# Performance work log

Hardware: AMD Instinct MI355X
Metric: run time of the kernel (lower is better)

Reference implementation:

```python
import jax, jax.numpy as jnp
import numpy as np

B, T, D_MODEL, HEAD_DIM = 8, 2048, 1024, 128


def setup_inputs() -> dict:
    key = jax.random.key(0)
    k1, k2, k3, k4 = jax.random.split(key, 4)
    scale = 1.0 / np.sqrt(D_MODEL)
    return {
        "x": jax.random.normal(k1, (B, T, D_MODEL), dtype=jnp.float32),
        "Wq": jax.random.normal(k2, (HEAD_DIM, D_MODEL), dtype=jnp.float32) * scale,
        "Wk": jax.random.normal(k3, (HEAD_DIM, D_MODEL), dtype=jnp.float32) * scale,
        "Wv": jax.random.normal(k4, (HEAD_DIM, D_MODEL), dtype=jnp.float32) * scale,
    }


def reference(x, Wq, Wk, Wv) -> jnp.ndarray:
    # x: [B, T, C]; torch Linear(no bias): y = x @ W.T, W: [head_dim, d_model]
    q = jnp.einsum("btc,hc->bth", x, Wq)  # [B, T, H]
    k = jnp.einsum("btc,hc->bth", x, Wk)
    v = jnp.einsum("btc,hc->bth", x, Wv)
    head_dim = Wq.shape[0]
    scores = jnp.einsum("bqh,bkh->bqk", q, k) / jnp.sqrt(jnp.float32(head_dim))  # [B, T, T]
    T_ = x.shape[1]
    causal = jnp.tril(jnp.ones((T_, T_), dtype=bool))
    scores = jnp.where(causal, scores, -jnp.inf)
    probs = jax.nn.softmax(scores, axis=-1)
    # dropout is identity at inference (eval mode)
    out = jnp.einsum("bqk,bkh->bqh", probs, v)  # [B, T, head_dim]
    return out
```

## Files before the change

kernel.cpp:

```cpp
#include <hip/hip_runtime.h>
#include <hip/hip_bf16.h>
#include <math.h>

#define T_ 2048
#define C_ 1024
#define H_ 128
#define NB 8
#define WN 131072
#define SC 0.08838834764831845f

typedef __attribute__((ext_vector_type(8))) short bf16x8;
typedef __attribute__((ext_vector_type(8))) unsigned short u16x8;
typedef __attribute__((ext_vector_type(4))) float f32x4;

#define MFMA16(a,b,c) __builtin_amdgcn_mfma_f32_16x16x32_bf16((a),(b),(c),0,0,0)

__device__ __forceinline__ unsigned short f2bf(float f) {
    union { float f; unsigned u; } v; v.f = f;
    unsigned r = v.u + 0x7fffu + ((v.u >> 16) & 1u);
    return (unsigned short)(r >> 16);
}
__device__ __forceinline__ float bf2f(unsigned short u) {
    union { unsigned u; float f; } v; v.u = ((unsigned)u) << 16; return v.f;
}
__device__ __forceinline__ unsigned pk2bf(float a, float b) {
    __hip_bfloat162 h = __float22bfloat162_rn(float2{a, b});
    union { __hip_bfloat162 h; unsigned u; } v; v.h = h; return v.u;
}
__device__ __forceinline__ void gld16(void* lds, const void* g) {
    __builtin_amdgcn_global_load_lds(
        (const __attribute__((address_space(1))) unsigned*)g,
        (__attribute__((address_space(3))) unsigned*)lds, 16, 0, 0);
}

__global__ __launch_bounds__(256) void wconv(const float* __restrict__ Wq,
                                             const float* __restrict__ Wk,
                                             const float* __restrict__ Wv,
                                             unsigned short* __restrict__ Wb) {
    int e = (blockIdx.x * 256 + threadIdx.x) * 8;
    int which = e >> 17;
    int off = e & (WN - 1);
    const float* src = (which == 0) ? Wq : (which == 1 ? Wk : Wv);
    float s = (which == 0) ? SC : 1.0f;
    const float4* p = (const float4*)(src + off);
    float4 a = p[0], b = p[1];
    uint4 o = { pk2bf(a.x * s, a.y * s), pk2bf(a.z * s, a.w * s),
                pk2bf(b.x * s, b.y * s), pk2bf(b.z * s, b.w * s) };
    *(uint4*)(Wb + e) = o;
}

__global__ __launch_bounds__(256, 2) void proj(const float* __restrict__ x,
                                               const unsigned short* __restrict__ Wb,
                                               unsigned short* __restrict__ Q,
                                               unsigned short* __restrict__ K,
                                               unsigned short* __restrict__ V) {
    __shared__ unsigned short Xs[2][32][40];
    __shared__ unsigned short Ws[2][384][32];

    const int tid  = threadIdx.x;
    const int wave = tid >> 6, lane = tid & 63;
    const int quad = lane >> 4, l16 = lane & 15;
    const int m0   = blockIdx.x * 32;

    f32x4 acc[2][6];
    #pragma unroll
    for (int i = 0; i < 2; i++)
        #pragma unroll
        for (int j = 0; j < 6; j++) acc[i][j] = {0.f, 0.f, 0.f, 0.f};

    const int xrow = tid >> 3, xc4 = (tid & 7) * 4;
    const float* xg = x + (size_t)(m0 + xrow) * C_ + xc4;
    const unsigned short* wg = Wb + (size_t)(wave * 96 + (lane >> 2)) * C_
                               + (size_t)(((lane & 3) ^ ((lane >> 3) & 3)) * 8);

    #define STAGE(buf, kc) do {                                                   \
        _Pragma("unroll")                                                         \
        for (int rb = 0; rb < 6; rb++)                                            \
            gld16(&Ws[buf][wave * 96 + rb * 16][0],                               \
                  wg + (size_t)rb * 16 * C_ + (kc));                              \
        float4 f = *(const float4*)(xg + (kc));                                   \
        *(uint2*)&Xs[buf][xrow][xc4] = uint2{ pk2bf(f.x, f.y), pk2bf(f.z, f.w) }; \
    } while (0)

    STAGE(0, 0);
    for (int it = 0; it < 32; it++) {
        __syncthreads();
        if (it < 31) { STAGE((it + 1) & 1, (it + 1) * 32); }
        const int buf = it & 1;
        bf16x8 af[2];
        af[0] = *(bf16x8*)&Xs[buf][l16][quad * 8];
        af[1] = *(bf16x8*)&Xs[buf][16 + l16][quad * 8];
        const int rsw = (l16 >> 1) & 3;
        #pragma unroll
        for (int nf = 0; nf < 6; nf++) {
            int row = wave * 96 + nf * 16 + l16;
            bf16x8 bq = *(bf16x8*)&Ws[buf][row][(quad ^ rsw) * 8];
            acc[0][nf] = MFMA16(af[0], bq, acc[0][nf]);
            acc[1][nf] = MFMA16(af[1], bq, acc[1][nf]);
        }
    }
    #undef STAGE

    #pragma unroll
    for (int nf = 0; nf < 6; nf++) {
        int nb = wave * 96 + nf * 16;
        int which = nb >> 7;
        unsigned short* dst = (which == 0) ? Q : (which == 1 ? K : V);
        int c = (nb & 127) + l16;
        #pragma unroll
        for (int mf = 0; mf < 2; mf++)
            #pragma unroll
            for (int r = 0; r < 4; r++)
                dst[(size_t)(m0 + mf * 16 + quad * 4 + r) * H_ + c] = f2bf(acc[mf][nf][r]);
    }
}

__global__ __launch_bounds__(256, 3) void attn(const unsigned short* __restrict__ Qg,
                                               const unsigned short* __restrict__ Kg,
                                               const unsigned short* __restrict__ Vg,
                                               unsigned short* __restrict__ Ob,
                                               float* __restrict__ Ml) {
    const int bx = blockIdx.x;
    const int s  = bx & 7, qt = 31 - (bx >> 3);
    const int b  = blockIdx.y;
    const int qbase = qt * 64, kstart = s * 256;
    if (kstart > qbase) return;
    const int kend  = (kstart + 256 < qbase + 64) ? kstart + 256 : qbase + 64;
    const int niter = (kend - kstart) >> 6;

    __shared__ unsigned short Ks[4][64][32];
    __shared__ unsigned short Vt[128 * 64];
    __shared__ unsigned short Ps[4][16][64];

    const int tid = threadIdx.x, wave = tid >> 6, lane = tid & 63;
    const int quad = lane >> 4, l16 = lane & 15;
    const size_t base = (size_t)b * T_ * H_;

    const unsigned short* ksrc = Kg + base + (size_t)(kstart + (lane >> 2)) * H_ + wave * 32 + (lane & 3) * 8;
    #pragma unroll
    for (int p = 0; p < 4; p++) gld16(&Ks[wave][p * 16][0], ksrc + (size_t)p * 16 * H_);
    const unsigned short* vsrc = Vg + base + (size_t)(kstart + wave * 8 + quad * 2) * H_ + l16 * 8;
    u16x8 vr[2][2];
    vr[0][0] = *(const u16x8*)vsrc;             vr[0][1] = *(const u16x8*)(vsrc + H_);
    vr[1][0] = *(const u16x8*)(vsrc + 32 * H_); vr[1][1] = *(const u16x8*)(vsrc + 33 * H_);

    bf16x8 qf[4];
    const unsigned short* qp = Qg + base + (size_t)(qbase + wave * 16 + l16) * H_ + quad * 8;
    #pragma unroll
    for (int kk = 0; kk < 4; kk++) qf[kk] = *(const bf16x8*)(qp + kk * 32);

    f32x4 o[8];
    #pragma unroll
    for (int i = 0; i < 8; i++) o[i] = {0.f, 0.f, 0.f, 0.f};
    float m_i = -INFINITY, l_i = 0.f;
    const int swz = (l16 & 7) << 3;
    const int qg = qbase + wave * 16 + l16;

    __syncthreads();

    #pragma unroll
    for (int g = 0; g < 2; g++) {
        int t0 = wave * 8 + g * 32 + quad * 2;
        int t8 = t0 >> 3;
        #pragma unroll
        for (int j = 0; j < 8; j++) {
            int h = l16 * 8 + j;
            unsigned pk = (unsigned)(unsigned short)vr[g][0][j] | ((unsigned)(unsigned short)vr[g][1][j] << 16);
            int blk = (t8 ^ (h & 7) ^ ((h >> 3) & 7)) & 7;
            *(unsigned*)&Vt[h * 64 + blk * 8 + (t0 & 7)] = pk;
        }
    }

    for (int kt = 0; ; kt++) {
        const int kbase = kstart + kt * 64;
        f32x4 st[4];
        #pragma unroll
        for (int nf = 0; nf < 4; nf++) st[nf] = {0.f, 0.f, 0.f, 0.f};
        #pragma unroll
        for (int kk = 0; kk < 4; kk++)
            #pragma unroll
            for (int nf = 0; nf < 4; nf++) {
                bf16x8 kfr = *(bf16x8*)&Ks[kk][nf * 16 + l16][quad * 8];
                st[nf] = MFMA16(kfr, qf[kk], st[nf]);
            }
        if (kbase + 64 > qbase) {
            #pragma unroll
            for (int nf = 0; nf < 4; nf++) {
                int kg = kbase + nf * 16 + quad * 4;
                #pragma unroll
                for (int r = 0; r < 4; r++)
                    if (kg + r > qg) st[nf][r] = -INFINITY;
            }
        }
        float mx = st[0][0];
        #pragma unroll
        for (int nf = 0; nf < 4; nf++)
            #pragma unroll
            for (int r = 0; r < 4; r++) mx = fmaxf(mx, st[nf][r]);
        mx = fmaxf(mx, __shfl_xor(mx, 16, 64));
        mx = fmaxf(mx, __shfl_xor(mx, 32, 64));
        float mnew = fmaxf(m_i, mx);
        float al = __expf(m_i - mnew);
        m_i = mnew;
        float rs = 0.f;
        #pragma unroll
        for (int nf = 0; nf < 4; nf++)
            #pragma unroll
            for (int r = 0; r < 4; r++) {
                float e = __expf(st[nf][r] - mnew);
                st[nf][r] = e; rs += e;
            }
        rs += __shfl_xor(rs, 16, 64);
        rs += __shfl_xor(rs, 32, 64);
        l_i = al * l_i + rs;
        #pragma unroll
        for (int nf = 0; nf < 4; nf++) {
            uint2 pk = { pk2bf(st[nf][0], st[nf][1]), pk2bf(st[nf][2], st[nf][3]) };
            *(uint2*)&Ps[wave][l16][(nf * 16 + quad * 4) ^ swz] = pk;
        }
        float a0 = __shfl(al, quad * 4 + 0, 64), a1 = __shfl(al, quad * 4 + 1, 64);
        float a2 = __shfl(al, quad * 4 + 2, 64), a3 = __shfl(al, quad * 4 + 3, 64);
        #pragma unroll
        for (int i = 0; i < 8; i++) {
            o[i][0] *= a0; o[i][1] *= a1; o[i][2] *= a2; o[i][3] *= a3;
        }
        __syncthreads();

        const bool more = (kt + 1 < niter);
        if (more) {
            ksrc += 64 * H_;
            #pragma unroll
            for (int p = 0; p < 4; p++) gld16(&Ks[wave][p * 16][0], ksrc + (size_t)p * 16 * H_);
            vsrc += 64 * H_;
            vr[0][0] = *(const u16x8*)vsrc;             vr[0][1] = *(const u16x8*)(vsrc + H_);
            vr[1][0] = *(const u16x8*)(vsrc + 32 * H_); vr[1][1] = *(const u16x8*)(vsrc + 33 * H_);
        }
        bf16x8 pa0 = *(bf16x8*)&Ps[wave][l16][(quad * 8) ^ swz];
        bf16x8 pa1 = *(bf16x8*)&Ps[wave][l16][(32 + quad * 8) ^ swz];
        #pragma unroll
        for (int nf = 0; nf < 8; nf++) {
            int h = nf * 16 + l16;
            int ex = (h & 7) ^ ((h >> 3) & 7);
            bf16x8 v0 = *(bf16x8*)&Vt[h * 64 + ((quad ^ ex) & 7) * 8];
            bf16x8 v1 = *(bf16x8*)&Vt[h * 64 + (((quad + 4) ^ ex) & 7) * 8];
            o[nf] = MFMA16(pa0, v0, o[nf]);
            o[nf] = MFMA16(pa1, v1, o[nf]);
        }
        if (!more) break;
        __syncthreads();
        #pragma unroll
        for (int g = 0; g < 2; g++) {
            int t0 = wave * 8 + g * 32 + quad * 2;
            int t8 = t0 >> 3;
            #pragma unroll
            for (int j = 0; j < 8; j++) {
                int h = l16 * 8 + j;
                unsigned pk = (unsigned)(unsigned short)vr[g][0][j] | ((unsigned)(unsigned short)vr[g][1][j] << 16);
                int blk = (t8 ^ (h & 7) ^ ((h >> 3) & 7)) & 7;
                *(unsigned*)&Vt[h * 64 + blk * 8 + (t0 & 7)] = pk;
            }
        }
    }

    const int g2 = qt >> 2;
    const int Pq = 2 * g2 * (g2 + 1) + (qt & 3) * (g2 + 1);
    const int slot = (Pq + s) * NB + b;
    float lq[4];
    #pragma unroll
    for (int r = 0; r < 4; r++) lq[r] = __shfl(l_i, quad * 4 + r, 64);
    const size_t obase = (size_t)slot * 64 * 128;
    #pragma unroll
    for (int r = 0; r < 4; r++) {
        float invl = 1.0f / lq[r];
        #pragma unroll
        for (int nf = 0; nf < 8; nf++)
            Ob[obase + (size_t)(wave * 16 + quad * 4 + r) * 128 + nf * 16 + l16] = f2bf(o[nf][r] * invl);
    }
    if (lane < 16) {
        int ridx = slot * 64 + wave * 16 + l16;
        Ml[ridx * 2]     = m_i;
        Ml[ridx * 2 + 1] = l_i;
    }
}

__global__ __launch_bounds__(256) void merge(const unsigned short* __restrict__ Ob,
                                             const float* __restrict__ Ml,
                                             float* __restrict__ out) {
    const int qt = blockIdx.x, b = blockIdx.y;
    const int g = qt >> 2;
    const int Pq = 2 * g * (g + 1) + (qt & 3) * (g + 1);
    const int ns = g + 1;
    const int tid = threadIdx.x;
    const int row = tid >> 2, c0 = (tid & 3) * 32;

    float mv[8], lv[8], mg = -INFINITY;
    for (int s2 = 0; s2 < ns; s2++) {
        int slot = (Pq + s2) * NB + b;
        mv[s2] = Ml[(slot * 64 + row) * 2];
        lv[s2] = Ml[(slot * 64 + row) * 2 + 1];
        mg = fmaxf(mg, mv[s2]);
    }
    float L = 0.f, w[8];
    for (int s2 = 0; s2 < ns; s2++) { w[s2] = lv[s2] * __expf(mv[s2] - mg); L += w[s2]; }
    float inv = 1.0f / L;

    float accv[32];
    #pragma unroll
    for (int i = 0; i < 32; i++) accv[i] = 0.f;
    for (int s2 = 0; s2 < ns; s2++) {
        int slot = (Pq + s2) * NB + b;
        const unsigned short* op = Ob + ((size_t)(slot * 64 + row)) * 128 + c0;
        #pragma unroll
        for (int cc = 0; cc < 4; cc++) {
            u16x8 v = *(const u16x8*)(op + cc * 8);
            #pragma unroll
            for (int j = 0; j < 8; j++) accv[cc * 8 + j] += w[s2] * bf2f(v[j]);
        }
    }
    float* od = out + ((size_t)(b * T_ + qt * 64 + row)) * 128 + c0;
    #pragma unroll
    for (int cc = 0; cc < 8; cc++) {
        float4 w4 = { accv[cc*4] * inv, accv[cc*4+1] * inv, accv[cc*4+2] * inv, accv[cc*4+3] * inv };
        *(float4*)(od + cc * 4) = w4;
    }
}

extern "C" void kernel_launch(void* const* d_in, const int* in_sizes, int n_in,
                              void* d_out, int out_size, void* d_ws, size_t ws_size,
                              hipStream_t stream) {
    const float* x  = (const float*)d_in[0];
    const float* Wq = (const float*)d_in[1];
    const float* Wk = (const float*)d_in[2];
    const float* Wv = (const float*)d_in[3];

    char* ws = (char*)d_ws;
    unsigned short* Wb = (unsigned short*)ws;
    unsigned short* Q  = (unsigned short*)(ws + (size_t) 1 * (1u << 20));
    unsigned short* K  = (unsigned short*)(ws + (size_t) 5 * (1u << 20));
    unsigned short* V  = (unsigned short*)(ws + (size_t) 9 * (1u << 20));
    unsigned short* Ob = (unsigned short*)(ws + (size_t)13 * (1u << 20));
    float*          Ml = (float*)(ws + (size_t)32 * (1u << 20));
    float* out = (float*)d_out;

    hipLaunchKernelGGL(wconv, dim3(192), dim3(256), 0, stream, Wq, Wk, Wv, Wb);
    hipLaunchKernelGGL(proj,  dim3(512), dim3(256), 0, stream, x, Wb, Q, K, V);
    hipLaunchKernelGGL(attn,  dim3(256, NB), dim3(256), 0, stream, Q, K, V, Ob, Ml);
    hipLaunchKernelGGL(merge, dim3(32, NB), dim3(256), 0, stream, Ob, Ml, out);
}
```

Measured before the change: 181.7 us.

## Retile QKV projection to 64x192 blocks with K=64 steps and deferred X conversion

The projection kernel now gives each block a 64-row by 192-column output tile, using a 2x2 wave grid and 64-wide K slices with XOR-swizzled shared memory. This halves the number of K iterations, and each loaded X tile is reused across more output columns per wave. The fp32 X loads are issued before the MFMAs and converted and stored to shared memory afterwards, so their global latency overlaps compute. In exchange, each block re-reads X for both column halves, and it uses more shared memory and registers, which may reduce occupancy.

Measured after the change: 175.0 us. 3.7% less time.

```diff
diff --git a/kernel.cpp b/kernel.cpp
--- a/kernel.cpp
+++ b/kernel.cpp
@@ -54,13 +54,15 @@
                                                unsigned short* __restrict__ Q,
                                                unsigned short* __restrict__ K,
                                                unsigned short* __restrict__ V) {
-    __shared__ unsigned short Xs[2][32][40];
-    __shared__ unsigned short Ws[2][384][32];
+    __shared__ unsigned short Xs[2][64][64];
+    __shared__ unsigned short Ws[2][192][64];
 
     const int tid  = threadIdx.x;
     const int wave = tid >> 6, lane = tid & 63;
     const int quad = lane >> 4, l16 = lane & 15;
-    const int m0   = blockIdx.x * 32;
+    const int wm   = wave >> 1, wn = wave & 1;
+    const int m0   = (blockIdx.x >> 1) * 64;
+    const int n0   = (blockIdx.x & 1) * 192;
 
     f32x4 acc[2][6];
     #pragma unroll
@@ -68,42 +70,62 @@
         #pragma unroll
         for (int j = 0; j < 6; j++) acc[i][j] = {0.f, 0.f, 0.f, 0.f};
 
-    const int xrow = tid >> 3, xc4 = (tid & 7) * 4;
-    const float* xg = x + (size_t)(m0 + xrow) * C_ + xc4;
-    const unsigned short* wg = Wb + (size_t)(wave * 96 + (lane >> 2)) * C_
-                               + (size_t)(((lane & 3) ^ ((lane >> 3) & 3)) * 8);
-
-    #define STAGE(buf, kc) do {                                                   \
+    const int xrow = tid >> 2, xcg = tid & 3;
+    const float* xg = x + (size_t)(m0 + xrow) * C_ + xcg * 16;
+    const int xk = xrow & 7;
+    const unsigned short* wg = Wb + (size_t)(n0 + wave * 48 + (lane >> 3)) * C_
+                               + (size_t)(((lane & 7) ^ (lane >> 3)) * 8);
+
+    float4 xr0, xr1, xr2, xr3;
+    #define ISSUE(buf, kc) do {                                                   \
         _Pragma("unroll")                                                         \
-        for (int rb = 0; rb < 6; rb++)                                            \
-            gld16(&Ws[buf][wave * 96 + rb * 16][0],                               \
-                  wg + (size_t)rb * 16 * C_ + (kc));                              \
-        float4 f = *(const float4*)(xg + (kc));                                   \
-        *(uint2*)&Xs[buf][xrow][xc4] = uint2{ pk2bf(f.x, f.y), pk2bf(f.z, f.w) }; \
+        for (int i = 0; i < 6; i++)                                               \
+            gld16(&Ws[buf][wave * 48 + i * 8][0], wg + (size_t)i * 8 * C_ + (kc));\
+        const float* xp = xg + (kc);                                              \
+        xr0 = *(const float4*)xp;        xr1 = *(const float4*)(xp + 4);          \
+        xr2 = *(const float4*)(xp + 8);  xr3 = *(const float4*)(xp + 12);         \
     } while (0)
 
-    STAGE(0, 0);
-    for (int it = 0; it < 32; it++) {
+    #define XWRITE(buf) do {                                                      \
+        uint4 u0 = { pk2bf(xr0.x, xr0.y), pk2bf(xr0.z, xr0.w),                    \
+                     pk2bf(xr1.x, xr1.y), pk2bf(xr1.z, xr1.w) };                  \
+        uint4 u1 = { pk2bf(xr2.x, xr2.y), pk2bf(xr2.z, xr2.w),                    \
+                     pk2bf(xr3.x, xr3.y), pk2bf(xr3.z, xr3.w) };                  \
+        *(uint4*)&Xs[buf][xrow][((2 * xcg)     ^ xk) * 8] = u0;                   \
+        *(uint4*)&Xs[buf][xrow][((2 * xcg + 1) ^ xk) * 8] = u1;                   \
+    } while (0)
+
+    ISSUE(0, 0);
+    XWRITE(0);
+    for (int it = 0; it < 16; it++) {
         __syncthreads();
-        if (it < 31) { STAGE((it + 1) & 1, (it + 1) * 32); }
         const int buf = it & 1;
-        bf16x8 af[2];
-        af[0] = *(bf16x8*)&Xs[buf][l16][quad * 8];
-        af[1] = *(bf16x8*)&Xs[buf][16 + l16][quad * 8];
-        const int rsw = (l16 >> 1) & 3;
-        #pragma unroll
-        for (int nf = 0; nf < 6; nf++) {
-            int row = wave * 96 + nf * 16 + l16;
-            bf16x8 bq = *(bf16x8*)&Ws[buf][row][(quad ^ rsw) * 8];
-            acc[0][nf] = MFMA16(af[0], bq, acc[0][nf]);
-            acc[1][nf] = MFMA16(af[1], bq, acc[1][nf]);
-        }
-    }
-    #undef STAGE
+        if (it < 15) ISSUE(buf ^ 1, (it + 1) * 64);
+        const int key = l16 & 7;
+        bf16x8 af[2][2];
+        #pragma unroll
+        for (int kk = 0; kk < 2; kk++)
+            #pragma unroll
+            for (int mf = 0; mf < 2; mf++)
+                af[mf][kk] = *(bf16x8*)&Xs[buf][wm * 32 + mf * 16 + l16]
+                                          [((kk * 4 + quad) ^ key) * 8];
+        #pragma unroll
+        for (int kk = 0; kk < 2; kk++)
+            #pragma unroll
+            for (int nf = 0; nf < 6; nf++) {
+                bf16x8 bq = *(bf16x8*)&Ws[buf][wn * 96 + nf * 16 + l16]
+                                         [((kk * 4 + quad) ^ key) * 8];
+                acc[0][nf] = MFMA16(af[0][kk], bq, acc[0][nf]);
+                acc[1][nf] = MFMA16(af[1][kk], bq, acc[1][nf]);
+            }
+        if (it < 15) XWRITE(buf ^ 1);
+    }
+    #undef ISSUE
+    #undef XWRITE
 
     #pragma unroll
     for (int nf = 0; nf < 6; nf++) {
-        int nb = wave * 96 + nf * 16;
+        int nb = n0 + wn * 96 + nf * 16;
         int which = nb >> 7;
         unsigned short* dst = (which == 0) ? Q : (which == 1 ? K : V);
         int c = (nb & 127) + l16;
@@ -111,7 +133,7 @@
         for (int mf = 0; mf < 2; mf++)
             #pragma unroll
             for (int r = 0; r < 4; r++)
-                dst[(size_t)(m0 + mf * 16 + quad * 4 + r) * H_ + c] = f2bf(acc[mf][nf][r]);
+                dst[(size_t)(m0 + wm * 32 + mf * 16 + quad * 4 + r) * H_ + c] = f2bf(acc[mf][nf][r]);
     }
 }
 
```
